# Performance work log

Measured on AMD Instinct MI355X. Metric: run time of the kernel, lower is better.

Reference implementation:

```python
import jax, jax.numpy as jnp
import numpy as np

D_EMB = 1024
B, T = 8, 2048

def setup_inputs() -> dict:
    key = jax.random.key(0)
    ks = jax.random.split(key, 7)
    s = 0.02
    return {
        "x": jax.random.normal(ks[0], (B, T, D_EMB), dtype=jnp.float32),
        "W_attn": jax.random.normal(ks[1], (3 * D_EMB, D_EMB), dtype=jnp.float32) * s,
        "b_attn": jax.random.normal(ks[2], (3 * D_EMB,), dtype=jnp.float32) * s,
        "W_proj": jax.random.normal(ks[3], (D_EMB, D_EMB), dtype=jnp.float32) * s,
        "b_proj": jax.random.normal(ks[4], (D_EMB,), dtype=jnp.float32) * s,
        "W_fc": jax.random.normal(ks[5], (1, D_EMB), dtype=jnp.float32) * s,
        "b_fc": jax.random.normal(ks[6], (1,), dtype=jnp.float32) * s,
    }

def reference(x, W_attn, b_attn, W_proj, b_proj, W_fc, b_fc):
    # qkv projection: torch Linear => x @ W.T + b
    qkv = jnp.einsum('btc,dc->btd', x, W_attn) + b_attn          # [B,T,3C]
    q, k, v = jnp.split(qkv, 3, axis=2)                          # each [B,T,C]
    scale = q.shape[-1] ** (-0.5)
    attn_scores = jnp.einsum('btc,bsc->bts', q, k) * scale       # [B,T,T]
    attn_weights = jax.nn.softmax(attn_scores, axis=-1)          # traditional softmax
    y = jnp.einsum('bts,bsc->btc', attn_weights, v)              # [B,T,C]
    y = jnp.einsum('btc,dc->btd', y, W_proj) + b_proj            # [B,T,C]
    out = jnp.einsum('btc,oc->bto', y, W_fc) + b_fc              # [B,T,1]
    return out
```

## Files before the change

### kernel.cpp

```cpp
#include <hip/hip_runtime.h>
#include <stdint.h>

#define D_EMB 1024
#define NBATCH 8
#define SEQ 2048
#define MTOT (NBATCH*SEQ)

typedef __attribute__((ext_vector_type(8))) short short8;
typedef __attribute__((ext_vector_type(4))) float f32x4;

__device__ __forceinline__ ushort bf16r(float x) {
  union { float f; uint32_t u; } c; c.f = x;
  return (ushort)((c.u + 0x7fffu + ((c.u >> 16) & 1u)) >> 16);
}

__device__ __forceinline__ void cp16(const ushort* g, ushort* l) {
  __builtin_amdgcn_global_load_lds(
      (const __attribute__((address_space(1))) void*)g,
      (__attribute__((address_space(3))) void*)l, 16, 0, 0);
}

__global__ __launch_bounds__(256) void cvt_all(
    const float4* __restrict__ x4, const float4* __restrict__ W4,
    const float4* __restrict__ wv4, const float* __restrict__ sc,
    ushort* __restrict__ xb, ushort* __restrict__ wqkb, float* __restrict__ vw) {
  int tid = threadIdx.x;
  if (blockIdx.x < 4096) {
    int wave = tid >> 6, lane = tid & 63;
    long row = (long)blockIdx.x * 4 + wave;
    const float4* xr = x4 + row * 256;
    ushort* xo = xb + row * D_EMB;
    float s = 0.f;
    #pragma unroll
    for (int i = 0; i < 4; i++) {
      int idx = lane + i * 64;
      float4 v = xr[idx];
      float4 w = wv4[idx];
      *(ushort4*)(xo + idx * 4) = make_ushort4(bf16r(v.x), bf16r(v.y), bf16r(v.z), bf16r(v.w));
      s += v.x * w.x + v.y * w.y + v.z * w.z + v.w * w.w;
    }
    #pragma unroll
    for (int off = 32; off; off >>= 1) s += __shfl_xor(s, off);
    if (lane == 0) vw[row] = s + sc[1];
  } else {
    long base = (long)(blockIdx.x - 4096) * 1024 + tid;
    #pragma unroll
    for (int i = 0; i < 4; i++) {
      long idx = base + i * 256;
      float4 v = W4[idx];
      *(ushort4*)(wqkb + idx * 4) = make_ushort4(bf16r(v.x), bf16r(v.y), bf16r(v.z), bf16r(v.w));
    }
  }
}

__global__ void init_kernel(const float* __restrict__ bp, const float* __restrict__ Wfc,
                            const float* __restrict__ bfc,
                            float* __restrict__ w_eff, float* __restrict__ wv_eff,
                            float* __restrict__ numden, float* __restrict__ sc) {
  int tid = threadIdx.x;
  int b = blockIdx.x;
  if (b == 0) { w_eff[tid] = 0.f; return; }
  if (b == 1) { wv_eff[tid] = 0.f; return; }
  if (b >= 3) { numden[(long)(b - 3) * 1024 + tid] = 0.f; return; }
  float v = bp[tid] * Wfc[tid];
  int lane = tid & 63, w = tid >> 6;
  #pragma unroll
  for (int off = 32; off; off >>= 1) v += __shfl_xor(v, off);
  __shared__ float red[16];
  if (lane == 0) red[w] = v;
  __syncthreads();
  if (tid == 0) {
    float s = 0.f;
    #pragma unroll
    for (int i = 0; i < 16; i++) s += red[i];
    sc[0] = s + bfc[0];
  }
}

__global__ void prep1(const float* __restrict__ Wp, const float* __restrict__ Wfc,
                      float* __restrict__ w_eff) {
  int c = blockIdx.x * 256 + threadIdx.x;
  int d0 = blockIdx.y * 16;
  float s = 0.f;
  #pragma unroll
  for (int d = d0; d < d0 + 16; d++) s += Wfc[d] * Wp[(long)d * D_EMB + c];
  atomicAdd(&w_eff[c], s);
}

__global__ void prep2(const float* __restrict__ Wattn, const float* __restrict__ battn,
                      const float* __restrict__ w_eff, float* __restrict__ wv_eff,
                      float* __restrict__ sc) {
  int tid = threadIdx.x;
  if (blockIdx.y == 64) {
    if (blockIdx.x != 0) return;
    float v = 0.f;
    #pragma unroll
    for (int i = 0; i < 4; i++) { int c = tid + i * 256; v += battn[2048 + c] * w_eff[c]; }
    int lane = tid & 63, w = tid >> 6;
    #pragma unroll
    for (int off = 32; off; off >>= 1) v += __shfl_xor(v, off);
    __shared__ float red[4];
    if (lane == 0) red[w] = v;
    __syncthreads();
    if (tid == 0) sc[1] = red[0] + red[1] + red[2] + red[3];
    return;
  }
  int d = blockIdx.x * 256 + tid;
  int c0 = blockIdx.y * 16;
  float s = 0.f;
  #pragma unroll
  for (int c = c0; c < c0 + 16; c++) s += w_eff[c] * Wattn[(long)(2048 + c) * D_EMB + d];
  atomicAdd(&wv_eff[d], s);
}

template<bool FUSED, bool REMAP>
__global__ __launch_bounds__(256, 4) void gemm_nt(
    const ushort* __restrict__ A, long lda, long sAz,
    const ushort* __restrict__ B, long ldb, long sBz,
    ushort* __restrict__ C, long ldc,
    const float* __restrict__ bias, float scale, int K,
    const float* __restrict__ vw, float* __restrict__ num, float* __restrict__ den) {
  __shared__ __align__(16) ushort lds_a[128 * 64];
  __shared__ __align__(16) ushort lds_b[128 * 64];

  int bx, by, z;
  if (REMAP) {
    long f = blockIdx.x + 16L * blockIdx.y + (FUSED ? 256L * blockIdx.z : 0L);
    int xcd = (int)(f & 7);
    long g = f >> 3;
    bx = (int)(g & 15);
    if (FUSED) { z = xcd; by = (int)(g >> 4); }
    else       { z = 0;   by = xcd * 16 + (int)(g >> 4); }
  } else {
    bx = blockIdx.x; by = blockIdx.y; z = blockIdx.z;
  }

  const ushort* Az = A + (long)z * sAz;
  const ushort* Bz = B + (long)z * sBz;
  long m0 = (long)by * 128, n0 = (long)bx * 128;
  int t = threadIdx.x;
  int wave = t >> 6, lane = t & 63;
  int r = lane & 15, q = lane >> 4;
  int wm = (wave & 1) * 64, wn = (wave >> 1) * 64;

  f32x4 acc[4][4] = {};

  int row0 = t >> 3;
  int kc = (t & 7) ^ (row0 & 7);
  const ushort* Ap = Az + (m0 + row0) * lda + kc * 8;
  const ushort* Bp = Bz + (n0 + row0) * ldb + kc * 8;
  long a32 = 32 * lda, b32 = 32 * ldb;

  int swz = r & 7;

  #pragma unroll 1
  for (int k0 = 0; k0 < K; k0 += 64) {
    if (k0) __syncthreads();
    cp16(Ap + k0,            lds_a + t * 8);
    cp16(Ap + k0 + a32,      lds_a + (t + 256) * 8);
    cp16(Ap + k0 + 2 * a32,  lds_a + (t + 512) * 8);
    cp16(Ap + k0 + 3 * a32,  lds_a + (t + 768) * 8);
    cp16(Bp + k0,            lds_b + t * 8);
    cp16(Bp + k0 + b32,      lds_b + (t + 256) * 8);
    cp16(Bp + k0 + 2 * b32,  lds_b + (t + 512) * 8);
    cp16(Bp + k0 + 3 * b32,  lds_b + (t + 768) * 8);
    __syncthreads();
    #pragma unroll
    for (int kk = 0; kk < 2; kk++) {
      int cidx = (kk * 4 + q) ^ swz;
      short8 af[4], bf[4];
      #pragma unroll
      for (int i = 0; i < 4; i++)
        af[i] = *(const short8*)(lds_a + ((wm + i * 16 + r) * 8 + cidx) * 8);
      #pragma unroll
      for (int j = 0; j < 4; j++)
        bf[j] = *(const short8*)(lds_b + ((wn + j * 16 + r) * 8 + cidx) * 8);
      #pragma unroll
      for (int i = 0; i < 4; i++)
        #pragma unroll
        for (int j = 0; j < 4; j++)
          acc[i][j] = __builtin_amdgcn_mfma_f32_16x16x32_bf16(af[i], bf[j], acc[i][j], 0, 0, 0);
    }
  }

  if (!FUSED) {
    #pragma unroll
    for (int i = 0; i < 4; i++) {
      #pragma unroll
      for (int j = 0; j < 4; j++) {
        long col = n0 + wn + j * 16 + r;
        float bj = bias[col];
        #pragma unroll
        for (int rr = 0; rr < 4; rr++) {
          long row = m0 + wm + i * 16 + q * 4 + rr;
          C[row * ldc + col] = bf16r(acc[i][j][rr] * scale + bj);
        }
      }
    }
  } else {
    const float* vwz = vw + (long)z * SEQ + n0;
    float* numz = num + (long)z * SEQ + m0;
    float* denz = den + (long)z * SEQ + m0;
    float vwj[4];
    #pragma unroll
    for (int j = 0; j < 4; j++) vwj[j] = vwz[wn + j * 16 + r];
    #pragma unroll
    for (int i = 0; i < 4; i++) {
      #pragma unroll
      for (int rr = 0; rr < 4; rr++) {
        float sn = 0.f, sd = 0.f;
        #pragma unroll
        for (int j = 0; j < 4; j++) {
          float e = __expf(acc[i][j][rr] * scale);
          sd += e;
          sn += e * vwj[j];
        }
        #pragma unroll
        for (int off = 1; off < 16; off <<= 1) {
          sn += __shfl_xor(sn, off);
          sd += __shfl_xor(sd, off);
        }
        if (r == 0) {
          int row = wm + i * 16 + q * 4 + rr;
          atomicAdd(&numz[row], sn);
          atomicAdd(&denz[row], sd);
        }
      }
    }
  }
}

__global__ __launch_bounds__(256) void finalize(
    const float* __restrict__ num, const float* __restrict__ den,
    const float* __restrict__ sc, float* __restrict__ out) {
  long i = blockIdx.x * 256L + threadIdx.x;
  out[i] = num[i] / den[i] + sc[0];
}

extern "C" void kernel_launch(void* const* d_in, const int* in_sizes, int n_in,
                              void* d_out, int out_size, void* d_ws, size_t ws_size,
                              hipStream_t stream) {
  const float* x     = (const float*)d_in[0];
  const float* Wattn = (const float*)d_in[1];
  const float* battn = (const float*)d_in[2];
  const float* Wproj = (const float*)d_in[3];
  const float* bproj = (const float*)d_in[4];
  const float* Wfc   = (const float*)d_in[5];
  const float* bfc   = (const float*)d_in[6];
  float* out = (float*)d_out;

  const size_t OFF_XB    = 0;
  const size_t OFF_WQKB  = 33554432;
  const size_t OFF_QK    = 37748736;
  const size_t OFF_NUM   = 104857600;
  const size_t OFF_DEN   = 104923136;
  const size_t OFF_VW    = 104988672;
  const size_t OFF_WEFF  = 105054208;
  const size_t OFF_WVEFF = 105058304;
  const size_t OFF_SC    = 105062400;
  const size_t NEED      = 105062408;
  if (ws_size < NEED) return;

  char* ws = (char*)d_ws;
  ushort* xb    = (ushort*)(ws + OFF_XB);
  ushort* wqkb  = (ushort*)(ws + OFF_WQKB);
  ushort* qk    = (ushort*)(ws + OFF_QK);
  float* num    = (float*)(ws + OFF_NUM);
  float* den    = (float*)(ws + OFF_DEN);
  float* vw     = (float*)(ws + OFF_VW);
  float* w_eff  = (float*)(ws + OFF_WEFF);
  float* wv_eff = (float*)(ws + OFF_WVEFF);
  float* sc     = (float*)(ws + OFF_SC);

  init_kernel<<<dim3(35), dim3(1024), 0, stream>>>(bproj, Wfc, bfc, w_eff, wv_eff, num, sc);
  prep1<<<dim3(4, 64), dim3(256), 0, stream>>>(Wproj, Wfc, w_eff);
  prep2<<<dim3(4, 65), dim3(256), 0, stream>>>(Wattn, battn, w_eff, wv_eff, sc);

  cvt_all<<<dim3(4096 + 512), dim3(256), 0, stream>>>(
      (const float4*)x, (const float4*)Wattn, (const float4*)wv_eff, sc, xb, wqkb, vw);

  gemm_nt<false, true><<<dim3(16, 128, 1), dim3(256), 0, stream>>>(
      xb, (long)D_EMB, 0L, wqkb, (long)D_EMB, 0L,
      qk, 2048L, battn, 1.0f, D_EMB, nullptr, nullptr, nullptr);

  gemm_nt<true, false><<<dim3(16, 16, NBATCH), dim3(256), 0, stream>>>(
      qk, 2048L, (long)SEQ * 2048, qk + 1024, 2048L, (long)SEQ * 2048,
      nullptr, 0L, nullptr, 0.03125f, D_EMB, vw, num, den);

  finalize<<<dim3(64), dim3(256), 0, stream>>>(num, den, sc, out);
}
```

Measured before the change: 274.0 us.

## Enlarge GEMM tiles to 256x256 with 8 waves and multi-stage LDS pipeline

Both bf16 GEMMs now use 256x256 output tiles computed by 512 threads (8 waves, each holding 128x64 of accumulators). Global-to-LDS copies run through a 4-slot ring of half-k-tiles, so the next loads are issued before the MFMAs and waited on with explicit vmcnt counts instead of a full sync per k-step. The blocks also use s_setprio around the MFMA bursts and a new XCD remap for the 8x64 grid. This targets LDS/global load latency and per-tile overhead, at the cost of 128 KB of LDS per block, higher register pressure and fewer blocks in the grid (512 and 512).

After: 270.7 us. No clear change (-1.2%).

```diff
diff --git a/kernel.cpp b/kernel.cpp
--- a/kernel.cpp
+++ b/kernel.cpp
@@ -114,86 +114,105 @@
 }
 
 template<bool FUSED, bool REMAP>
-__global__ __launch_bounds__(256, 4) void gemm_nt(
+__global__ __launch_bounds__(512, 2) void gemm_nt(
     const ushort* __restrict__ A, long lda, long sAz,
     const ushort* __restrict__ B, long ldb, long sBz,
     ushort* __restrict__ C, long ldc,
     const float* __restrict__ bias, float scale, int K,
     const float* __restrict__ vw, float* __restrict__ num, float* __restrict__ den) {
-  __shared__ __align__(16) ushort lds_a[128 * 64];
-  __shared__ __align__(16) ushort lds_b[128 * 64];
+  __shared__ __align__(16) ushort lds[65536];
 
   int bx, by, z;
   if (REMAP) {
-    long f = blockIdx.x + 16L * blockIdx.y + (FUSED ? 256L * blockIdx.z : 0L);
-    int xcd = (int)(f & 7);
-    long g = f >> 3;
-    bx = (int)(g & 15);
-    if (FUSED) { z = xcd; by = (int)(g >> 4); }
-    else       { z = 0;   by = xcd * 16 + (int)(g >> 4); }
+    int f = (int)(blockIdx.x + 8u * blockIdx.y);
+    int xcd = f & 7, g = f >> 3;
+    bx = g & 7; by = xcd * 8 + (g >> 3); z = 0;
   } else {
     bx = blockIdx.x; by = blockIdx.y; z = blockIdx.z;
   }
 
   const ushort* Az = A + (long)z * sAz;
   const ushort* Bz = B + (long)z * sBz;
-  long m0 = (long)by * 128, n0 = (long)bx * 128;
+  long m0 = (long)by * 256, n0 = (long)bx * 256;
   int t = threadIdx.x;
   int wave = t >> 6, lane = t & 63;
   int r = lane & 15, q = lane >> 4;
-  int wm = (wave & 1) * 64, wn = (wave >> 1) * 64;
-
-  f32x4 acc[4][4] = {};
-
-  int row0 = t >> 3;
-  int kc = (t & 7) ^ (row0 & 7);
-  const ushort* Ap = Az + (m0 + row0) * lda + kc * 8;
-  const ushort* Bp = Bz + (n0 + row0) * ldb + kc * 8;
-  long a32 = 32 * lda, b32 = 32 * ldb;
-
-  int swz = r & 7;
-
-  #pragma unroll 1
-  for (int k0 = 0; k0 < K; k0 += 64) {
-    if (k0) __syncthreads();
-    cp16(Ap + k0,            lds_a + t * 8);
-    cp16(Ap + k0 + a32,      lds_a + (t + 256) * 8);
-    cp16(Ap + k0 + 2 * a32,  lds_a + (t + 512) * 8);
-    cp16(Ap + k0 + 3 * a32,  lds_a + (t + 768) * 8);
-    cp16(Bp + k0,            lds_b + t * 8);
-    cp16(Bp + k0 + b32,      lds_b + (t + 256) * 8);
-    cp16(Bp + k0 + 2 * b32,  lds_b + (t + 512) * 8);
-    cp16(Bp + k0 + 3 * b32,  lds_b + (t + 768) * 8);
-    __syncthreads();
-    #pragma unroll
-    for (int kk = 0; kk < 2; kk++) {
-      int cidx = (kk * 4 + q) ^ swz;
-      short8 af[4], bf[4];
-      #pragma unroll
-      for (int i = 0; i < 4; i++)
-        af[i] = *(const short8*)(lds_a + ((wm + i * 16 + r) * 8 + cidx) * 8);
+  int wm = wave >> 2, wn = wave & 3;
+
+  f32x4 acc[8][4] = {};
+
+  int srow0 = t >> 2, srow1 = srow0 + 128;
+  int scs = t & 3;
+  const ushort* pA0 = Az + (m0 + srow0) * lda + (long)((scs ^ ((srow0 >> 1) & 3)) * 8);
+  const ushort* pA1 = Az + (m0 + srow1) * lda + (long)((scs ^ ((srow1 >> 1) & 3)) * 8);
+  const ushort* pB0 = Bz + (n0 + srow0) * ldb + (long)((scs ^ ((srow0 >> 1) & 3)) * 8);
+  const ushort* pB1 = Bz + (n0 + srow1) * ldb + (long)((scs ^ ((srow1 >> 1) & 3)) * 8);
+  ushort* ldsA = lds;
+  ushort* ldsB = lds + 32768;
+  int d0 = t * 8, d1 = (t + 512) * 8;
+
+  int swz8 = (q ^ ((r >> 1) & 3)) * 8;
+  int offa = (wm * 128 + r) * 32 + swz8;
+  int offb = (wn * 64 + r) * 32 + swz8;
+
+  int NT = K >> 6;
+  int SMAX = 2 * NT;
+
+#define STAGE(tile_, kk_) do { \
+    long ko_ = (long)(tile_) * 64 + (long)(kk_) * 32; \
+    int rg_ = (((tile_) & 1) * 2 + (kk_)) * 8192; \
+    cp16(pA0 + ko_, ldsA + rg_ + d0); \
+    cp16(pA1 + ko_, ldsA + rg_ + d1); \
+    cp16(pB0 + ko_, ldsB + rg_ + d0); \
+    cp16(pB1 + ko_, ldsB + rg_ + d1); \
+  } while (0)
+
+  STAGE(0, 0); STAGE(0, 1); STAGE(1, 0);
+  asm volatile("s_waitcnt vmcnt(8)" ::: "memory");
+  __builtin_amdgcn_s_barrier();
+
+  #pragma unroll 4
+  for (int s = 0; s < SMAX; ++s) {
+    int reg = (((s >> 1) & 1) * 2 + (s & 1)) * 8192;
+    short8 af[8], bfr[4];
+    #pragma unroll
+    for (int fr = 0; fr < 8; fr++)
+      af[fr] = *(const short8*)(ldsA + reg + offa + fr * 512);
+    #pragma unroll
+    for (int j = 0; j < 4; j++)
+      bfr[j] = *(const short8*)(ldsB + reg + offb + j * 512);
+
+    int stile = (s + 3) >> 1;
+    if (stile < NT) STAGE(stile, (s + 3) & 1);
+
+    __builtin_amdgcn_s_barrier();
+    asm volatile("s_waitcnt lgkmcnt(0)" ::: "memory");
+    __builtin_amdgcn_s_setprio(1);
+    #pragma unroll
+    for (int fr = 0; fr < 8; fr++)
       #pragma unroll
       for (int j = 0; j < 4; j++)
-        bf[j] = *(const short8*)(lds_b + ((wn + j * 16 + r) * 8 + cidx) * 8);
-      #pragma unroll
-      for (int i = 0; i < 4; i++)
-        #pragma unroll
-        for (int j = 0; j < 4; j++)
-          acc[i][j] = __builtin_amdgcn_mfma_f32_16x16x32_bf16(af[i], bf[j], acc[i][j], 0, 0, 0);
-    }
-  }
+        acc[fr][j] = __builtin_amdgcn_mfma_f32_16x16x32_bf16(af[fr], bfr[j], acc[fr][j], 0, 0, 0);
+    __builtin_amdgcn_s_setprio(0);
+
+    if (s < SMAX - 3)       asm volatile("s_waitcnt vmcnt(6)" ::: "memory");
+    else if (s == SMAX - 3) asm volatile("s_waitcnt vmcnt(4)" ::: "memory");
+    else if (s == SMAX - 2) asm volatile("s_waitcnt vmcnt(0)" ::: "memory");
+    __builtin_amdgcn_s_barrier();
+  }
+#undef STAGE
 
   if (!FUSED) {
     #pragma unroll
-    for (int i = 0; i < 4; i++) {
+    for (int fr = 0; fr < 8; fr++) {
       #pragma unroll
       for (int j = 0; j < 4; j++) {
-        long col = n0 + wn + j * 16 + r;
+        long col = n0 + wn * 64 + j * 16 + r;
         float bj = bias[col];
         #pragma unroll
         for (int rr = 0; rr < 4; rr++) {
-          long row = m0 + wm + i * 16 + q * 4 + rr;
-          C[row * ldc + col] = bf16r(acc[i][j][rr] * scale + bj);
+          long row = m0 + wm * 128 + fr * 16 + q * 4 + rr;
+          C[row * ldc + col] = bf16r(acc[fr][j][rr] * scale + bj);
         }
       }
     }
@@ -203,15 +222,15 @@
     float* denz = den + (long)z * SEQ + m0;
     float vwj[4];
     #pragma unroll
-    for (int j = 0; j < 4; j++) vwj[j] = vwz[wn + j * 16 + r];
-    #pragma unroll
-    for (int i = 0; i < 4; i++) {
+    for (int j = 0; j < 4; j++) vwj[j] = vwz[wn * 64 + j * 16 + r];
+    #pragma unroll
+    for (int fr = 0; fr < 8; fr++) {
       #pragma unroll
       for (int rr = 0; rr < 4; rr++) {
         float sn = 0.f, sd = 0.f;
         #pragma unroll
         for (int j = 0; j < 4; j++) {
-          float e = __expf(acc[i][j][rr] * scale);
+          float e = __expf(acc[fr][j][rr] * scale);
           sd += e;
           sn += e * vwj[j];
         }
@@ -221,7 +240,7 @@
           sd += __shfl_xor(sd, off);
         }
         if (r == 0) {
-          int row = wm + i * 16 + q * 4 + rr;
+          int row = wm * 128 + fr * 16 + q * 4 + rr;
           atomicAdd(&numz[row], sn);
           atomicAdd(&denz[row], sd);
         }
@@ -279,11 +298,11 @@
   cvt_all<<<dim3(4096 + 512), dim3(256), 0, stream>>>(
       (const float4*)x, (const float4*)Wattn, (const float4*)wv_eff, sc, xb, wqkb, vw);
 
-  gemm_nt<false, true><<<dim3(16, 128, 1), dim3(256), 0, stream>>>(
+  gemm_nt<false, true><<<dim3(8, 64, 1), dim3(512), 0, stream>>>(
       xb, (long)D_EMB, 0L, wqkb, (long)D_EMB, 0L,
       qk, 2048L, battn, 1.0f, D_EMB, nullptr, nullptr, nullptr);
 
-  gemm_nt<true, false><<<dim3(16, 16, NBATCH), dim3(256), 0, stream>>>(
+  gemm_nt<true, false><<<dim3(8, 8, NBATCH), dim3(512), 0, stream>>>(
       qk, 2048L, (long)SEQ * 2048, qk + 1024, 2048L, (long)SEQ * 2048,
       nullptr, 0L, nullptr, 0.03125f, D_EMB, vw, num, den);
 
```

## Fold Wq^T Wk into a precomputed matrix to halve the projection GEMM

Applied to the files above, without the earlier changes.

Precomputes M = Wk^T·Wq (bf16) from a transposed copy of the attention weights and projects x once through M, so scores become (xM)·x instead of q·k. The q-bias contribution on keys is folded into a per-key additive term bb computed alongside the x conversion, and t-only terms are dropped since softmax cancels them. This halves the first GEMM's output width and removes the qk intermediate, at the cost of an extra 1024^3 GEMM and extra bf16 rounding of M.

Result: faster. 260.8 us (-4.8%).

```diff
diff --git a/kernel.cpp b/kernel.cpp
--- a/kernel.cpp
+++ b/kernel.cpp
@@ -20,71 +20,76 @@
       (__attribute__((address_space(3))) void*)l, 16, 0, 0);
 }
 
-__global__ __launch_bounds__(256) void cvt_all(
-    const float4* __restrict__ x4, const float4* __restrict__ W4,
-    const float4* __restrict__ wv4, const float* __restrict__ sc,
-    ushort* __restrict__ xb, ushort* __restrict__ wqkb, float* __restrict__ vw) {
-  int tid = threadIdx.x;
-  if (blockIdx.x < 4096) {
-    int wave = tid >> 6, lane = tid & 63;
-    long row = (long)blockIdx.x * 4 + wave;
-    const float4* xr = x4 + row * 256;
-    ushort* xo = xb + row * D_EMB;
-    float s = 0.f;
-    #pragma unroll
-    for (int i = 0; i < 4; i++) {
-      int idx = lane + i * 64;
-      float4 v = xr[idx];
-      float4 w = wv4[idx];
-      *(ushort4*)(xo + idx * 4) = make_ushort4(bf16r(v.x), bf16r(v.y), bf16r(v.z), bf16r(v.w));
-      s += v.x * w.x + v.y * w.y + v.z * w.z + v.w * w.w;
-    }
-    #pragma unroll
-    for (int off = 32; off; off >>= 1) s += __shfl_xor(s, off);
-    if (lane == 0) vw[row] = s + sc[1];
-  } else {
-    long base = (long)(blockIdx.x - 4096) * 1024 + tid;
-    #pragma unroll
-    for (int i = 0; i < 4; i++) {
-      long idx = base + i * 256;
-      float4 v = W4[idx];
-      *(ushort4*)(wqkb + idx * 4) = make_ushort4(bf16r(v.x), bf16r(v.y), bf16r(v.z), bf16r(v.w));
-    }
-  }
-}
-
-__global__ void init_kernel(const float* __restrict__ bp, const float* __restrict__ Wfc,
-                            const float* __restrict__ bfc,
-                            float* __restrict__ w_eff, float* __restrict__ wv_eff,
-                            float* __restrict__ numden, float* __restrict__ sc) {
+__global__ __launch_bounds__(256) void cvt_w(
+    const float4* __restrict__ Wattn4, const float* __restrict__ bproj,
+    const float* __restrict__ Wfc, const float* __restrict__ bfc,
+    ushort* __restrict__ wt, float* __restrict__ w_eff, float* __restrict__ wv_eff,
+    float* __restrict__ v_eff, float4* __restrict__ numden4, float* __restrict__ sc) {
   int tid = threadIdx.x;
   int b = blockIdx.x;
-  if (b == 0) { w_eff[tid] = 0.f; return; }
-  if (b == 1) { wv_eff[tid] = 0.f; return; }
-  if (b >= 3) { numden[(long)(b - 3) * 1024 + tid] = 0.f; return; }
-  float v = bp[tid] * Wfc[tid];
-  int lane = tid & 63, w = tid >> 6;
-  #pragma unroll
-  for (int off = 32; off; off >>= 1) v += __shfl_xor(v, off);
-  __shared__ float red[16];
-  if (lane == 0) red[w] = v;
-  __syncthreads();
-  if (tid == 0) {
+  __shared__ ushort lt[64][68];
+  __shared__ float red[4];
+  if (b < 512) {
+    int td = b & 31, tc = b >> 5;
+    #pragma unroll
+    for (int rep = 0; rep < 4; rep++) {
+      int i = (tid >> 4) + rep * 16;
+      int jj = tid & 15;
+      float4 v = Wattn4[(long)(td * 64 + i) * 256 + tc * 16 + jj];
+      lt[i][jj * 4 + 0] = bf16r(v.x);
+      lt[i][jj * 4 + 1] = bf16r(v.y);
+      lt[i][jj * 4 + 2] = bf16r(v.z);
+      lt[i][jj * 4 + 3] = bf16r(v.w);
+    }
+    __syncthreads();
+    #pragma unroll
+    for (int rep = 0; rep < 2; rep++) {
+      int c = (tid >> 3) + rep * 32;
+      int d0 = (tid & 7) * 8;
+      short8 o;
+      #pragma unroll
+      for (int k = 0; k < 8; k++) o[k] = (short)lt[d0 + k][c];
+      *(short8*)(wt + (long)(tc * 64 + c) * 2048 + td * 64 + d0) = o;
+    }
+    return;
+  }
+  int b2 = b - 512;
+  if (b2 == 0) {
+    for (int i = tid; i < 1024; i += 256) { w_eff[i] = 0.f; wv_eff[i] = 0.f; v_eff[i] = 0.f; }
+    return;
+  }
+  if (b2 == 1) {
+    float v = 0.f;
+    #pragma unroll
+    for (int i = 0; i < 4; i++) { int c = tid + i * 256; v += bproj[c] * Wfc[c]; }
+    int lane = tid & 63, w = tid >> 6;
+    #pragma unroll
+    for (int off = 32; off; off >>= 1) v += __shfl_xor(v, off);
+    if (lane == 0) red[w] = v;
+    __syncthreads();
+    if (tid == 0) sc[0] = red[0] + red[1] + red[2] + red[3] + bfc[0];
+    return;
+  }
+  numden4[(long)(b2 - 2) * 256 + tid] = make_float4(0.f, 0.f, 0.f, 0.f);
+}
+
+__global__ void prep1(const float* __restrict__ Wp, const float* __restrict__ Wfc,
+                      const float* __restrict__ Wattn, const float* __restrict__ battn,
+                      float* __restrict__ w_eff, float* __restrict__ v_eff) {
+  int c = blockIdx.x * 256 + threadIdx.x;
+  if (blockIdx.y < 64) {
+    int d0 = blockIdx.y * 16;
     float s = 0.f;
     #pragma unroll
-    for (int i = 0; i < 16; i++) s += red[i];
-    sc[0] = s + bfc[0];
-  }
-}
-
-__global__ void prep1(const float* __restrict__ Wp, const float* __restrict__ Wfc,
-                      float* __restrict__ w_eff) {
-  int c = blockIdx.x * 256 + threadIdx.x;
-  int d0 = blockIdx.y * 16;
-  float s = 0.f;
-  #pragma unroll
-  for (int d = d0; d < d0 + 16; d++) s += Wfc[d] * Wp[(long)d * D_EMB + c];
-  atomicAdd(&w_eff[c], s);
+    for (int d = d0; d < d0 + 16; d++) s += Wfc[d] * Wp[(long)d * D_EMB + c];
+    atomicAdd(&w_eff[c], s);
+  } else {
+    int d0 = (blockIdx.y - 64) * 16;
+    float s = 0.f;
+    #pragma unroll
+    for (int d = d0; d < d0 + 16; d++) s += battn[d] * Wattn[(long)(1024 + d) * D_EMB + c];
+    atomicAdd(&v_eff[c], s);
+  }
 }
 
 __global__ void prep2(const float* __restrict__ Wattn, const float* __restrict__ battn,
@@ -113,28 +118,14 @@
   atomicAdd(&wv_eff[d], s);
 }
 
-template<bool FUSED, bool REMAP>
-__global__ __launch_bounds__(256, 4) void gemm_nt(
+template<int MODE>
+__device__ __forceinline__ void gemm_body(
+    int bx, int by, int z, ushort* lds_a, ushort* lds_b,
     const ushort* __restrict__ A, long lda, long sAz,
     const ushort* __restrict__ B, long ldb, long sBz,
-    ushort* __restrict__ C, long ldc,
-    const float* __restrict__ bias, float scale, int K,
-    const float* __restrict__ vw, float* __restrict__ num, float* __restrict__ den) {
-  __shared__ __align__(16) ushort lds_a[128 * 64];
-  __shared__ __align__(16) ushort lds_b[128 * 64];
-
-  int bx, by, z;
-  if (REMAP) {
-    long f = blockIdx.x + 16L * blockIdx.y + (FUSED ? 256L * blockIdx.z : 0L);
-    int xcd = (int)(f & 7);
-    long g = f >> 3;
-    bx = (int)(g & 15);
-    if (FUSED) { z = xcd; by = (int)(g >> 4); }
-    else       { z = 0;   by = xcd * 16 + (int)(g >> 4); }
-  } else {
-    bx = blockIdx.x; by = blockIdx.y; z = blockIdx.z;
-  }
-
+    ushort* __restrict__ C, long ldc, float scale, int K,
+    const float* __restrict__ vw, const float* __restrict__ bb,
+    float* __restrict__ num, float* __restrict__ den) {
   const ushort* Az = A + (long)z * sAz;
   const ushort* Bz = B + (long)z * sBz;
   long m0 = (long)by * 128, n0 = (long)bx * 128;
@@ -183,27 +174,30 @@
     }
   }
 
-  if (!FUSED) {
+  if (MODE == 0) {
     #pragma unroll
     for (int i = 0; i < 4; i++) {
       #pragma unroll
       for (int j = 0; j < 4; j++) {
         long col = n0 + wn + j * 16 + r;
-        float bj = bias[col];
         #pragma unroll
         for (int rr = 0; rr < 4; rr++) {
           long row = m0 + wm + i * 16 + q * 4 + rr;
-          C[row * ldc + col] = bf16r(acc[i][j][rr] * scale + bj);
+          C[row * ldc + col] = bf16r(acc[i][j][rr] * scale);
         }
       }
     }
   } else {
     const float* vwz = vw + (long)z * SEQ + n0;
+    const float* bbz = bb + (long)z * SEQ + n0;
     float* numz = num + (long)z * SEQ + m0;
     float* denz = den + (long)z * SEQ + m0;
-    float vwj[4];
-    #pragma unroll
-    for (int j = 0; j < 4; j++) vwj[j] = vwz[wn + j * 16 + r];
+    float vwj[4], bbj[4];
+    #pragma unroll
+    for (int j = 0; j < 4; j++) {
+      vwj[j] = vwz[wn + j * 16 + r];
+      bbj[j] = bbz[wn + j * 16 + r];
+    }
     #pragma unroll
     for (int i = 0; i < 4; i++) {
       #pragma unroll
@@ -211,7 +205,7 @@
         float sn = 0.f, sd = 0.f;
         #pragma unroll
         for (int j = 0; j < 4; j++) {
-          float e = __expf(acc[i][j][rr] * scale);
+          float e = __expf((acc[i][j][rr] + bbj[j]) * scale);
           sd += e;
           sn += e * vwj[j];
         }
@@ -230,6 +224,62 @@
   }
 }
 
+__global__ __launch_bounds__(256, 4) void cvt_mt(
+    const float4* __restrict__ x4, const float4* __restrict__ wv4,
+    const float4* __restrict__ v4, const float* __restrict__ sc,
+    ushort* __restrict__ xb, float* __restrict__ vw, float* __restrict__ bb,
+    const ushort* __restrict__ wt, ushort* __restrict__ mt) {
+  __shared__ __align__(16) ushort lds_a[128 * 64];
+  __shared__ __align__(16) ushort lds_b[128 * 64];
+  int tid = threadIdx.x;
+  if (blockIdx.x < 64) {
+    int b = blockIdx.x;
+    gemm_body<0>(b & 7, b >> 3, 0, lds_a, lds_b,
+                 wt + 1024, 2048L, 0L, wt, 2048L, 0L,
+                 mt, 1024L, 1.0f, D_EMB, nullptr, nullptr, nullptr, nullptr);
+    return;
+  }
+  int wave = tid >> 6, lane = tid & 63;
+  long row = (long)(blockIdx.x - 64) * 4 + wave;
+  const float4* xr = x4 + row * 256;
+  ushort* xo = xb + row * D_EMB;
+  float s = 0.f, s2 = 0.f;
+  #pragma unroll
+  for (int i = 0; i < 4; i++) {
+    int idx = lane + i * 64;
+    float4 v = xr[idx];
+    float4 w = wv4[idx];
+    float4 u = v4[idx];
+    *(ushort4*)(xo + idx * 4) = make_ushort4(bf16r(v.x), bf16r(v.y), bf16r(v.z), bf16r(v.w));
+    s  += v.x * w.x + v.y * w.y + v.z * w.z + v.w * w.w;
+    s2 += v.x * u.x + v.y * u.y + v.z * u.z + v.w * u.w;
+  }
+  #pragma unroll
+  for (int off = 32; off; off >>= 1) { s += __shfl_xor(s, off); s2 += __shfl_xor(s2, off); }
+  if (lane == 0) { vw[row] = s + sc[1]; bb[row] = s2; }
+}
+
+template<int MODE, int RMODE>
+__global__ __launch_bounds__(256, 4) void gemm_nt(
+    const ushort* __restrict__ A, long lda, long sAz,
+    const ushort* __restrict__ B, long ldb, long sBz,
+    ushort* __restrict__ C, long ldc, float scale, int K,
+    const float* __restrict__ vw, const float* __restrict__ bb,
+    float* __restrict__ num, float* __restrict__ den) {
+  __shared__ __align__(16) ushort lds_a[128 * 64];
+  __shared__ __align__(16) ushort lds_b[128 * 64];
+  int bx, by, z;
+  if (RMODE == 1) {
+    int f = (int)(blockIdx.x + 8u * blockIdx.y);
+    int xcd = f & 7, g = f >> 3;
+    by = xcd * 16 + (g & 15); bx = g >> 4; z = 0;
+  } else {
+    bx = blockIdx.x; by = blockIdx.y; z = blockIdx.z;
+  }
+  gemm_body<MODE>(bx, by, z, lds_a, lds_b, A, lda, sAz, B, ldb, sBz,
+                  C, ldc, scale, K, vw, bb, num, den);
+}
+
 __global__ __launch_bounds__(256) void finalize(
     const float* __restrict__ num, const float* __restrict__ den,
     const float* __restrict__ sc, float* __restrict__ out) {
@@ -250,42 +300,51 @@
   float* out = (float*)d_out;
 
   const size_t OFF_XB    = 0;
-  const size_t OFF_WQKB  = 33554432;
-  const size_t OFF_QK    = 37748736;
-  const size_t OFF_NUM   = 104857600;
-  const size_t OFF_DEN   = 104923136;
-  const size_t OFF_VW    = 104988672;
-  const size_t OFF_WEFF  = 105054208;
-  const size_t OFF_WVEFF = 105058304;
-  const size_t OFF_SC    = 105062400;
-  const size_t NEED      = 105062408;
+  const size_t OFF_WT    = 33554432;
+  const size_t OFF_MT    = 37748736;
+  const size_t OFF_XM    = 39845888;
+  const size_t OFF_NUM   = 73400320;
+  const size_t OFF_DEN   = 73465856;
+  const size_t OFF_VW    = 73531392;
+  const size_t OFF_BB    = 73596928;
+  const size_t OFF_WEFF  = 73662464;
+  const size_t OFF_WVEFF = 73666560;
+  const size_t OFF_VEFF  = 73670656;
+  const size_t OFF_SC    = 73674752;
+  const size_t NEED      = 73674760;
   if (ws_size < NEED) return;
 
   char* ws = (char*)d_ws;
   ushort* xb    = (ushort*)(ws + OFF_XB);
-  ushort* wqkb  = (ushort*)(ws + OFF_WQKB);
-  ushort* qk    = (ushort*)(ws + OFF_QK);
+  ushort* wt    = (ushort*)(ws + OFF_WT);
+  ushort* mt    = (ushort*)(ws + OFF_MT);
+  ushort* xm    = (ushort*)(ws + OFF_XM);
   float* num    = (float*)(ws + OFF_NUM);
   float* den    = (float*)(ws + OFF_DEN);
   float* vw     = (float*)(ws + OFF_VW);
+  float* bb     = (float*)(ws + OFF_BB);
   float* w_eff  = (float*)(ws + OFF_WEFF);
   float* wv_eff = (float*)(ws + OFF_WVEFF);
+  float* v_eff  = (float*)(ws + OFF_VEFF);
   float* sc     = (float*)(ws + OFF_SC);
 
-  init_kernel<<<dim3(35), dim3(1024), 0, stream>>>(bproj, Wfc, bfc, w_eff, wv_eff, num, sc);
-  prep1<<<dim3(4, 64), dim3(256), 0, stream>>>(Wproj, Wfc, w_eff);
+  cvt_w<<<dim3(546), dim3(256), 0, stream>>>(
+      (const float4*)Wattn, bproj, Wfc, bfc, wt, w_eff, wv_eff, v_eff, (float4*)num, sc);
+
+  prep1<<<dim3(4, 128), dim3(256), 0, stream>>>(Wproj, Wfc, Wattn, battn, w_eff, v_eff);
+
   prep2<<<dim3(4, 65), dim3(256), 0, stream>>>(Wattn, battn, w_eff, wv_eff, sc);
 
-  cvt_all<<<dim3(4096 + 512), dim3(256), 0, stream>>>(
-      (const float4*)x, (const float4*)Wattn, (const float4*)wv_eff, sc, xb, wqkb, vw);
-
-  gemm_nt<false, true><<<dim3(16, 128, 1), dim3(256), 0, stream>>>(
-      xb, (long)D_EMB, 0L, wqkb, (long)D_EMB, 0L,
-      qk, 2048L, battn, 1.0f, D_EMB, nullptr, nullptr, nullptr);
-
-  gemm_nt<true, false><<<dim3(16, 16, NBATCH), dim3(256), 0, stream>>>(
-      qk, 2048L, (long)SEQ * 2048, qk + 1024, 2048L, (long)SEQ * 2048,
-      nullptr, 0L, nullptr, 0.03125f, D_EMB, vw, num, den);
+  cvt_mt<<<dim3(64 + 4096), dim3(256), 0, stream>>>(
+      (const float4*)x, (const float4*)wv_eff, (const float4*)v_eff, sc, xb, vw, bb, wt, mt);
+
+  gemm_nt<0, 1><<<dim3(8, 128, 1), dim3(256), 0, stream>>>(
+      xb, (long)D_EMB, 0L, mt, (long)D_EMB, 0L,
+      xm, (long)D_EMB, 1.0f, D_EMB, nullptr, nullptr, nullptr, nullptr);
+
+  gemm_nt<1, 0><<<dim3(16, 16, NBATCH), dim3(256), 0, stream>>>(
+      xm, (long)D_EMB, (long)SEQ * D_EMB, xb, (long)D_EMB, (long)SEQ * D_EMB,
+      nullptr, 0L, 0.03125f, D_EMB, vw, bb, num, den);
 
   finalize<<<dim3(64), dim3(256), 0, stream>>>(num, den, sc, out);
 }
```
